# Optimization experiments

Measured on AMD Instinct MI355X. Metric: run time of the kernel, lower is better.

The kernel has to match this reference:

```python
import jax, jax.numpy as jnp
import numpy as np

D = 768
NH = 8
HD = D // NH
LAT = 64


def layernorm(x, g, b, eps=1e-5):
    mu = x.mean(-1, keepdims=True)
    var = ((x - mu) ** 2).mean(-1, keepdims=True)
    return (x - mu) * jax.lax.rsqrt(var + eps) * g + b


def mha(q, k, v, qw, qb, kw, kb, vw, vb, ow, ob):
    # torch nn.MultiheadAttention (batch_first): Linear is x @ W.T + b
    B, Lq, _ = q.shape
    qh = (q @ qw.T + qb).reshape(B, Lq, NH, HD)
    kh = (k @ kw.T + kb).reshape(B, -1, NH, HD)
    vh = (v @ vw.T + vb).reshape(B, -1, NH, HD)
    s = jnp.einsum('bqhd,bkhd->bhqk', qh, kh) * (1.0 / np.sqrt(HD))
    a = jax.nn.softmax(s, axis=-1)
    o = jnp.einsum('bhqk,bkhd->bqhd', a, vh).reshape(B, Lq, D)
    return o @ ow.T + ob


def setup_inputs() -> dict:
    key = jax.random.key(0)
    ks = jax.random.split(key, 16)
    w = lambda k, shape: (jax.random.normal(k, shape, jnp.float32) * 0.02)
    inp = {
        'frames': jax.random.normal(ks[0], (4, 4, 8, 3, 224, 224), jnp.float32),
        'pe_w': w(ks[1], (D, 3, 14, 14)), 'pe_b': jnp.zeros((D,), jnp.float32),
        'latents': jax.random.normal(ks[2], (LAT, D), jnp.float32),
        'ca_qw': w(ks[3], (D, D)), 'ca_qb': jnp.zeros((D,), jnp.float32),
        'ca_kw': w(ks[4], (D, D)), 'ca_kb': jnp.zeros((D,), jnp.float32),
        'ca_vw': w(ks[5], (D, D)), 'ca_vb': jnp.zeros((D,), jnp.float32),
        'ca_ow': w(ks[6], (D, D)), 'ca_ob': jnp.zeros((D,), jnp.float32),
        'nq_g': jnp.ones((D,), jnp.float32), 'nq_b': jnp.zeros((D,), jnp.float32),
        'nkv_g': jnp.ones((D,), jnp.float32), 'nkv_b': jnp.zeros((D,), jnp.float32),
        'no_g': jnp.ones((D,), jnp.float32), 'no_b': jnp.zeros((D,), jnp.float32),
        'm1_w': w(ks[7], (4 * D, D)), 'm1_b': jnp.zeros((4 * D,), jnp.float32),
        'm2_w': w(ks[8], (D, 4 * D)), 'm2_b': jnp.zeros((D,), jnp.float32),
        'sa_qw': w(ks[9], (D, D)), 'sa_qb': jnp.zeros((D,), jnp.float32),
        'sa_kw': w(ks[10], (D, D)), 'sa_kb': jnp.zeros((D,), jnp.float32),
        'sa_vw': w(ks[11], (D, D)), 'sa_vb': jnp.zeros((D,), jnp.float32),
        'sa_ow': w(ks[12], (D, D)), 'sa_ob': jnp.zeros((D,), jnp.float32),
        'f1_w': w(ks[13], (2 * D, D)), 'f1_b': jnp.zeros((2 * D,), jnp.float32),
        'f2_w': w(ks[14], (D, 2 * D)), 'f2_b': jnp.zeros((D,), jnp.float32),
        'n1_g': jnp.ones((D,), jnp.float32), 'n1_b': jnp.zeros((D,), jnp.float32),
        'n2_g': jnp.ones((D,), jnp.float32), 'n2_b': jnp.zeros((D,), jnp.float32),
    }
    return inp


def reference(frames, pe_w, pe_b, latents, ca_qw, ca_qb, ca_kw, ca_kb, ca_vw, ca_vb,
              ca_ow, ca_ob, nq_g, nq_b, nkv_g, nkv_b, no_g, no_b, m1_w, m1_b, m2_w, m2_b,
              sa_qw, sa_qb, sa_kw, sa_kb, sa_vw, sa_vb, sa_ow, sa_ob, f1_w, f1_b,
              f2_w, f2_b, n1_g, n1_b, n2_g, n2_b):
    B, S, T, C, H, W = frames.shape
    # --- patch embed (Conv2d k=14 s=14), batched over all seconds & frames ---
    f = frames.reshape(B * S * T, C, H, W)
    p = jax.lax.conv_general_dilated(
        f, pe_w, window_strides=(14, 14), padding='VALID',
        dimension_numbers=('NCHW', 'OIHW', 'NCHW')) + pe_b[None, :, None, None]
    npatch = p.shape[2] * p.shape[3]  # 256 patches per frame
    p = p.reshape(B * S * T, D, npatch).transpose(0, 2, 1)  # [BST, P, D]
    kv = p.reshape(B * S, T * npatch, D)  # per-second patch tokens
    # --- Perceiver second tokenizer (loop over seconds == batched over B*S) ---
    q = jnp.broadcast_to(latents[None], (B * S, LAT, D))
    out = mha(layernorm(q, nq_g, nq_b), layernorm(kv, nkv_g, nkv_b), kv,
              ca_qw, ca_qb, ca_kw, ca_kb, ca_vw, ca_vb, ca_ow, ca_ob)
    h = layernorm(out, no_g, no_b)
    tok = out + (jax.nn.gelu(h @ m1_w.T + m1_b) @ m2_w.T + m2_b)
    # concat second tokens along time
    x = tok.reshape(B, S * LAT, D)
    # --- temporal_agg: TransformerEncoderLayer (post-norm, relu, eval mode) ---
    attn = mha(x, x, x, sa_qw, sa_qb, sa_kw, sa_kb, sa_vw, sa_vb, sa_ow, sa_ob)
    x = layernorm(x + attn, n1_g, n1_b)
    ff = jax.nn.relu(x @ f1_w.T + f1_b) @ f2_w.T + f2_b
    x = layernorm(x + ff, n2_g, n2_b)
    return x
```

## Files before the change

### kernel.cpp

```cpp
#include <hip/hip_runtime.h>
#include <hip/hip_bf16.h>
#include <math.h>

typedef __hip_bfloat16 bf16;
typedef __attribute__((ext_vector_type(8))) short short8;
typedef __attribute__((ext_vector_type(4))) short short4v;
typedef __attribute__((ext_vector_type(4))) float f32x4;

__device__ __forceinline__ void gload16(const bf16* g, bf16* l) {
  __builtin_amdgcn_global_load_lds((const __attribute__((address_space(1))) void*)(g),
                                   (__attribute__((address_space(3))) void*)(l), 16, 0, 0);
}
__device__ __forceinline__ float bfu2f(unsigned short u) {
  union { unsigned u; float f; } c; c.u = ((unsigned)u) << 16; return c.f;
}
__device__ __forceinline__ short bf2s(float v) {
  union { bf16 h; short s; } c; c.h = __float2bfloat16(v); return c.s;
}
__device__ __forceinline__ short4v packbf4(f32x4 v) {
  short4v o;
  o[0] = bf2s(v[0]); o[1] = bf2s(v[1]); o[2] = bf2s(v[2]); o[3] = bf2s(v[3]);
  return o;
}

struct Seg { const float* src; bf16* dst; int rows, sc, dc; const float* scale; };
struct Segs { Seg s[13]; };

__global__ __launch_bounds__(256) void preproc_kernel(
    Segs segs,
    const float* __restrict__ frames, bf16* __restrict__ imcol,
    const float* __restrict__ kw, const float* __restrict__ nkv_g,
    const float* __restrict__ nkv_b, const float* __restrict__ kb,
    float* __restrict__ s1, float* __restrict__ s2,
    const float* __restrict__ latents, const float* __restrict__ nq_g,
    const float* __restrict__ nq_b, bf16* __restrict__ q_ln,
    const float* __restrict__ ba, const float* __restrict__ bb,
    const float* __restrict__ bc, float* __restrict__ sab_cat) {
  __shared__ float red[16];
  int b = blockIdx.x, tid = threadIdx.x;
  if (b < 29952) {
    Seg sg = segs.s[b / 2304];
    int bx = b % 2304;
    long long total = (long long)sg.rows * sg.dc;
    for (long long idx = (long long)bx * 256 + tid; idx < total; idx += 2304LL * 256) {
      int r = (int)(idx / sg.dc), c = (int)(idx % sg.dc);
      float v = (c < sg.sc) ? sg.src[(long long)r * sg.sc + c] : 0.f;
      if (sg.scale && c < sg.sc) v *= sg.scale[c];
      sg.dst[idx] = __float2bfloat16(v);
    }
  } else if (b < 40192) {
    unsigned idx8 = (unsigned)(b - 29952) * 256u + tid;
    unsigned m = idx8 / 80u;
    unsigned k0 = (idx8 % 80u) * 8u;
    unsigned n = m >> 8;
    unsigned p = m & 255u;
    unsigned py = p >> 4, px = p & 15u;
    const float* fb = frames + ((size_t)n * 3u) * 224u * 224u +
                      (size_t)py * 14u * 224u + px * 14u;
    short8 o;
    #pragma unroll
    for (int e = 0; e < 8; ++e) {
      unsigned k = k0 + e;
      float v = 0.f;
      if (k < 588u) {
        unsigned c = k / 196u, r = k % 196u;
        unsigned i = r / 14u, j = r % 14u;
        v = fb[((size_t)c * 224u + i) * 224u + j];
      }
      o[e] = bf2s(v);
    }
    *(short8*)(imcol + (size_t)m * 640u + k0) = o;
  } else if (b < 40960) {
    int j = b - 40192;
    const float* wr_ = kw + (size_t)j * 768;
    float a = 0.f, c = 0.f;
    #pragma unroll
    for (int i = 0; i < 3; ++i) {
      int d = tid + i * 256;
      float wv = wr_[d];
      a += wv * nkv_g[d];
      c += wv * nkv_b[d];
    }
    for (int off = 32; off; off >>= 1) { a += __shfl_down(a, off); c += __shfl_down(c, off); }
    int w = tid >> 6;
    if ((tid & 63) == 0) { red[w] = a; red[8 + w] = c; }
    __syncthreads();
    if (tid == 0) {
      s1[j] = red[0] + red[1] + red[2] + red[3];
      s2[j] = red[8] + red[9] + red[10] + red[11] + kb[j];
    }
  } else if (b < 41088) {
    int row = b - 40960;
    size_t base = (size_t)row * 768;
    if (row >= 64) {
      for (int i = 0; i < 3; ++i) q_ln[base + tid + i * 256] = __float2bfloat16(0.f);
      return;
    }
    float x[3];
    for (int i = 0; i < 3; ++i) x[i] = latents[base + tid + i * 256];
    float s = x[0] + x[1] + x[2];
    float sq = x[0] * x[0] + x[1] * x[1] + x[2] * x[2];
    for (int off = 32; off; off >>= 1) {
      s += __shfl_down(s, off);
      sq += __shfl_down(sq, off);
    }
    int w = tid >> 6;
    if ((tid & 63) == 0) { red[w] = s; red[4 + w] = sq; }
    __syncthreads();
    if (tid == 0) {
      red[0] = red[0] + red[1] + red[2] + red[3];
      red[4] = red[4] + red[5] + red[6] + red[7];
    }
    __syncthreads();
    float mean = red[0] * (1.f / 768.f);
    float var = red[4] * (1.f / 768.f) - mean * mean;
    float rs = rsqrtf(var + 1e-5f);
    for (int i = 0; i < 3; ++i) {
      int c = tid + i * 256;
      q_ln[base + c] = __float2bfloat16((x[i] - mean) * rs * nq_g[c] + nq_b[c]);
    }
  } else {
    int i = (b - 41088) * 256 + tid;
    if (i < 2304)
      sab_cat[i] = i < 768 ? ba[i] : (i < 1536 ? bb[i - 768] : bc[i - 1536]);
  }
}

__global__ __launch_bounds__(256) void rowstats_kernel(const bf16* __restrict__ x,
                                                       float* __restrict__ mu,
                                                       float* __restrict__ rs) {
  int row = blockIdx.x * 4 + (threadIdx.x >> 6);
  int lane = threadIdx.x & 63;
  const unsigned short* p = (const unsigned short*)(x + (size_t)row * 768);
  float s = 0.f, sq = 0.f;
  #pragma unroll
  for (int i = 0; i < 3; ++i) {
    ushort4 v = *(const ushort4*)(p + lane * 4 + i * 256);
    float f0 = bfu2f(v.x), f1 = bfu2f(v.y), f2 = bfu2f(v.z), f3 = bfu2f(v.w);
    s += f0 + f1 + f2 + f3;
    sq += f0 * f0 + f1 * f1 + f2 * f2 + f3 * f3;
  }
  for (int off = 32; off; off >>= 1) { s += __shfl_down(s, off); sq += __shfl_down(sq, off); }
  if (lane == 0) {
    float m = s * (1.f / 768.f);
    float var = sq * (1.f / 768.f) - m * m;
    mu[row] = m;
    rs[row] = rsqrtf(var + 1e-5f);
  }
}

__global__ __launch_bounds__(256) void ln_kernel(const float* __restrict__ inF,
                                                 const bf16* __restrict__ inB,
                                                 const float* __restrict__ g,
                                                 const float* __restrict__ b,
                                                 float* __restrict__ outF,
                                                 bf16* __restrict__ outB,
                                                 int validRows) {
  int row = blockIdx.x;
  int tid = threadIdx.x;
  __shared__ float red[8];
  size_t base = (size_t)row * 768;
  if (row >= validRows) {
    for (int i = 0; i < 3; ++i) {
      int c = tid + i * 256;
      if (outB) outB[base + c] = __float2bfloat16(0.f);
      if (outF) outF[base + c] = 0.f;
    }
    return;
  }
  float x[3];
  for (int i = 0; i < 3; ++i) {
    int c = tid + i * 256;
    x[i] = inF ? inF[base + c] : __bfloat162float(inB[base + c]);
  }
  float s = x[0] + x[1] + x[2];
  float sq = x[0] * x[0] + x[1] * x[1] + x[2] * x[2];
  for (int off = 32; off; off >>= 1) {
    s += __shfl_down(s, off);
    sq += __shfl_down(sq, off);
  }
  int w = tid >> 6;
  if ((tid & 63) == 0) { red[w] = s; red[4 + w] = sq; }
  __syncthreads();
  if (tid == 0) {
    red[0] = red[0] + red[1] + red[2] + red[3];
    red[4] = red[4] + red[5] + red[6] + red[7];
  }
  __syncthreads();
  float mean = red[0] * (1.f / 768.f);
  float var = red[4] * (1.f / 768.f) - mean * mean;
  float rs = rsqrtf(var + 1e-5f);
  for (int i = 0; i < 3; ++i) {
    int c = tid + i * 256;
    float y = (x[i] - mean) * rs * g[c] + b[c];
    if (outF) outF[base + c] = y;
    if (outB) outB[base + c] = __float2bfloat16(y);
  }
}

__global__ __launch_bounds__(512, 2) void gemm256(
    const bf16* __restrict__ A, const bf16* __restrict__ Bw,
    const float* __restrict__ bias,
    bf16* __restrict__ outB,
    int M, int N, int K, int act,
    const float* __restrict__ rowMu, const float* __restrict__ rowRs,
    const float* __restrict__ s1, const float* __restrict__ s2,
    bf16* __restrict__ outB2) {
  __shared__ __align__(16) bf16 As[4][8192];
  __shared__ __align__(16) bf16 Bs[4][8192];
  int tid = threadIdx.x;
  int nwg = gridDim.x * gridDim.y;
  int orig = blockIdx.y * gridDim.x + blockIdx.x;
  int xcd = orig & 7, loc = orig >> 3;
  int qq = nwg >> 3, rr = nwg & 7;
  int swz = (xcd < rr) ? (xcd * (qq + 1) + loc) : (rr * (qq + 1) + (xcd - rr) * qq + loc);
  int m0 = (swz / gridDim.x) * 256, n0 = (swz % gridDim.x) * 256;

  int lane = tid & 63, w = tid >> 6;
  int wr = w >> 2, wc = w & 3;
  int l15 = lane & 15, lq = lane >> 4;

  f32x4 acc[8][4] = {};

  #define STAGEH(buf, kt, part)                                                \
    {                                                                          \
      int koct_ = w >> 1;                                                      \
      int row0_ = (w & 1) * 64 + ((part) & 1) * 128;                           \
      if ((part) < 2)                                                          \
        gload16(A + (size_t)(m0 + row0_ + lane) * K + (kt) + koct_ * 8,        \
                &As[buf][(koct_ * 256 + row0_) * 8]);                          \
      else                                                                     \
        gload16(Bw + (size_t)(n0 + row0_ + lane) * K + (kt) + koct_ * 8,       \
                &Bs[buf][(koct_ * 256 + row0_) * 8]);                          \
    }

  int T = K >> 5;
  #pragma unroll
  for (int p = 0; p < 4; ++p) STAGEH(0, 0, p);
  #pragma unroll
  for (int p = 0; p < 4; ++p) STAGEH(1, 32, p);
  STAGEH(2, 64, 0);
  STAGEH(2, 64, 1);
  asm volatile("s_waitcnt vmcnt(6)" ::: "memory");
  __builtin_amdgcn_s_barrier();

  for (int t = 0; t < T; ++t) {
    int bufc = t & 3, bufn2 = (t + 2) & 3, bufn3 = (t + 3) & 3;
    int kt2 = (t + 2) << 5, kt3 = (t + 3) << 5;
    short8 af[4], bfr[4];
    #pragma unroll
    for (int ni = 0; ni < 4; ++ni)
      bfr[ni] = *(const short8*)(&Bs[bufc][(lq * 256 + wc * 64 + ni * 16 + l15) * 8]);
    #pragma unroll
    for (int mi = 0; mi < 4; ++mi)
      af[mi] = *(const short8*)(&As[bufc][(lq * 256 + wr * 128 + mi * 16 + l15) * 8]);
    if (t + 2 < T) { STAGEH(bufn2, kt2, 2); STAGEH(bufn2, kt2, 3); }
    __builtin_amdgcn_s_barrier();
    asm volatile("" ::: "memory");
    __builtin_amdgcn_s_setprio(1);
    #pragma unroll
    for (int mi = 0; mi < 4; ++mi)
      #pragma unroll
      for (int ni = 0; ni < 4; ++ni)
        acc[mi][ni] = __builtin_amdgcn_mfma_f32_16x16x32_bf16(bfr[ni], af[mi],
                                                              acc[mi][ni], 0, 0, 0);
    __builtin_amdgcn_s_setprio(0);
    asm volatile("" ::: "memory");
    __builtin_amdgcn_s_barrier();
    #pragma unroll
    for (int mi = 0; mi < 4; ++mi)
      af[mi] = *(const short8*)(&As[bufc][(lq * 256 + wr * 128 + 64 + mi * 16 + l15) * 8]);
    if (t + 3 < T) { STAGEH(bufn3, kt3, 0); STAGEH(bufn3, kt3, 1); }
    if (t + 3 < T) {
      asm volatile("s_waitcnt vmcnt(6)" ::: "memory");
    } else if (t + 2 < T) {
      asm volatile("s_waitcnt vmcnt(4)" ::: "memory");
    } else if (t + 1 < T) {
      asm volatile("s_waitcnt vmcnt(0)" ::: "memory");
    }
    __builtin_amdgcn_s_barrier();
    asm volatile("" ::: "memory");
    __builtin_amdgcn_s_setprio(1);
    #pragma unroll
    for (int mi = 0; mi < 4; ++mi)
      #pragma unroll
      for (int ni = 0; ni < 4; ++ni)
        acc[4 + mi][ni] = __builtin_amdgcn_mfma_f32_16x16x32_bf16(bfr[ni], af[mi],
                                                                  acc[4 + mi][ni], 0, 0, 0);
    __builtin_amdgcn_s_setprio(0);
    asm volatile("" ::: "memory");
    __builtin_amdgcn_s_barrier();
  }
  #undef STAGEH

  bf16* ldsflat = (bf16*)As;
  bf16* ep = ldsflat + w * 1152;
  int rlo = lane >> 3, cg = lane & 7;

  if (act == 3) {
    int c0w = n0 + wc * 64;
    bool isV = (c0w < 768);
    bf16* dst = isV ? outB : outB2;
    int colbase = isV ? c0w : (c0w - 768);
    f32x4 bv[4], a1[4], a2[4];
    #pragma unroll
    for (int ni = 0; ni < 4; ++ni) {
      int cc = colbase + ni * 16 + lq * 4;
      if (isV) bv[ni] = *(const f32x4*)(bias + cc);
      else { a1[ni] = *(const f32x4*)(s1 + cc); a2[ni] = *(const f32x4*)(s2 + cc); }
    }
    #pragma unroll
    for (int mi = 0; mi < 8; ++mi) {
      int roww = m0 + wr * 128 + mi * 16 + l15;
      float rs_ = 0.f, mu_ = 0.f;
      if (!isV) { rs_ = rowRs[roww]; mu_ = rowMu[roww]; }
      #pragma unroll
      for (int ni = 0; ni < 4; ++ni) {
        f32x4 v;
        if (isV) v = acc[mi][ni] + bv[ni];
        else {
          #pragma unroll
          for (int j = 0; j < 4; ++j)
            v[j] = rs_ * (acc[mi][ni][j] - mu_ * a1[ni][j]) + a2[ni][j];
        }
        *(short4v*)(ep + l15 * 72 + ni * 16 + lq * 4) = packbf4(v);
      }
      asm volatile("s_waitcnt lgkmcnt(0)" ::: "memory");
      #pragma unroll
      for (int p = 0; p < 2; ++p) {
        int r = p * 8 + rlo;
        short8 d = *(const short8*)(ep + r * 72 + cg * 8);
        int rg = m0 + wr * 128 + mi * 16 + r;
        *(short8*)(dst + (size_t)rg * 768 + colbase + cg * 8) = d;
      }
      asm volatile("s_waitcnt lgkmcnt(0)" ::: "memory");
    }
    return;
  }

  {
    int c0w = n0 + wc * 64;
    f32x4 bv[4] = {};
    if (bias) {
      #pragma unroll
      for (int ni = 0; ni < 4; ++ni)
        bv[ni] = *(const f32x4*)(bias + c0w + ni * 16 + lq * 4);
    }
    #pragma unroll
    for (int mi = 0; mi < 8; ++mi) {
      #pragma unroll
      for (int ni = 0; ni < 4; ++ni) {
        f32x4 v = acc[mi][ni] + bv[ni];
        *(short4v*)(ep + l15 * 72 + ni * 16 + lq * 4) = packbf4(v);
      }
      asm volatile("s_waitcnt lgkmcnt(0)" ::: "memory");
      #pragma unroll
      for (int p = 0; p < 2; ++p) {
        int r = p * 8 + rlo;
        short8 d = *(const short8*)(ep + r * 72 + cg * 8);
        int rg = m0 + wr * 128 + mi * 16 + r;
        *(short8*)(outB + (size_t)rg * N + c0w + cg * 8) = d;
      }
      asm volatile("s_waitcnt lgkmcnt(0)" ::: "memory");
    }
  }
}

__global__ __launch_bounds__(256) void gemm_bf16(
    const bf16* __restrict__ A, const bf16* __restrict__ Bw,
    const float* __restrict__ bias, const float* __restrict__ resid,
    float* __restrict__ outF, bf16* __restrict__ outB,
    int M, int N, int K, int act) {
  __shared__ __align__(16) bf16 As[2][4096];
  __shared__ __align__(16) bf16 Bs[2][4096];
  int tid = threadIdx.x;
  int nwg = gridDim.x * gridDim.y;
  int orig = blockIdx.y * gridDim.x + blockIdx.x;
  int xcd = orig & 7, loc = orig >> 3;
  int qq = nwg >> 3, rr = nwg & 7;
  int swz = (xcd < rr) ? (xcd * (qq + 1) + loc) : (rr * (qq + 1) + (xcd - rr) * qq + loc);
  int m0 = (swz / gridDim.x) * 128, n0 = (swz % gridDim.x) * 128;

  int lane = tid & 63, w = tid >> 6;
  int wr = w >> 1, wc = w & 1;
  int l15 = lane & 15, lq = lane >> 4;
  const bf16* Abase = A + (size_t)m0 * K + w * 8;
  const bf16* Bbase = Bw + (size_t)n0 * K + w * 8;
  f32x4 acc[4][4] = {};

  int nt = K >> 5;
  #pragma unroll
  for (int i = 0; i < 2; ++i) {
    int r = i * 64 + lane;
    gload16(Abase + (size_t)r * K, &As[0][(w * 2 + i) * 512]);
    gload16(Bbase + (size_t)r * K, &Bs[0][(w * 2 + i) * 512]);
  }
  for (int t = 0; t < nt; ++t) {
    int cur = t & 1;
    if (t + 1 < nt) {
      int kt = (t + 1) << 5;
      #pragma unroll
      for (int i = 0; i < 2; ++i) {
        int r = i * 64 + lane;
        gload16(Abase + (size_t)r * K + kt, &As[cur ^ 1][(w * 2 + i) * 512]);
        gload16(Bbase + (size_t)r * K + kt, &Bs[cur ^ 1][(w * 2 + i) * 512]);
      }
      asm volatile("s_waitcnt vmcnt(4)" ::: "memory");
    } else {
      asm volatile("s_waitcnt vmcnt(0)" ::: "memory");
    }
    __builtin_amdgcn_s_barrier();
    asm volatile("" ::: "memory");
    const bf16* Ab = &As[cur][lq * 1024];
    const bf16* Bb = &Bs[cur][lq * 1024];
    short8 af[4], bfr[4];
    #pragma unroll
    for (int mi = 0; mi < 4; ++mi)
      af[mi] = *(const short8*)(Ab + (wr * 64 + mi * 16 + l15) * 8);
    #pragma unroll
    for (int ni = 0; ni < 4; ++ni)
      bfr[ni] = *(const short8*)(Bb + (wc * 64 + ni * 16 + l15) * 8);
    __builtin_amdgcn_s_setprio(1);
    #pragma unroll
    for (int mi = 0; mi < 4; ++mi)
      #pragma unroll
      for (int ni = 0; ni < 4; ++ni)
        acc[mi][ni] = __builtin_amdgcn_mfma_f32_16x16x32_bf16(bfr[ni], af[mi],
                                                              acc[mi][ni], 0, 0, 0);
    __builtin_amdgcn_s_setprio(0);
    asm volatile("" ::: "memory");
    __builtin_amdgcn_s_barrier();
  }

  #pragma unroll
  for (int ni = 0; ni < 4; ++ni) {
    int c0 = n0 + wc * 64 + ni * 16 + lq * 4;
    f32x4 bv = {};
    if (bias) bv = *(const f32x4*)(bias + c0);
    #pragma unroll
    for (int mi = 0; mi < 4; ++mi) {
      int row = m0 + wr * 64 + mi * 16 + l15;
      f32x4 v = acc[mi][ni] + bv;
      if (act == 1) {
        #pragma unroll
        for (int j = 0; j < 4; ++j) {
          float x = v[j];
          v[j] = 0.5f * x * (1.f + tanhf(0.79788456080286535f * (x + 0.044715f * x * x * x)));
        }
      } else if (act == 2) {
        #pragma unroll
        for (int j = 0; j < 4; ++j) v[j] = fmaxf(v[j], 0.f);
      }
      size_t idx = (size_t)row * N + c0;
      if (resid) v += *(const f32x4*)(resid + idx);
      if (outF) *(f32x4*)(outF + idx) = v;
      if (outB) *(short4v*)(outB + idx) = packbf4(v);
    }
  }
}

__global__ __launch_bounds__(256) void flash_kernel(
    const bf16* __restrict__ Q, const bf16* __restrict__ Kp,
    const bf16* __restrict__ V, bf16* __restrict__ O,
    int Lk, int qRPB, int kRPB, int oRPB, int ld) {
  const float scale = 0.10206207261596575f;
  __shared__ bf16 Vt[96 * 72];
  __shared__ bf16 Ps[4 * 16 * 72];
  int tid = threadIdx.x, lane = tid & 63, w = tid >> 6;
  int l15 = lane & 15, lq = lane >> 4;
  int b = blockIdx.z, h = blockIdx.y, qt = blockIdx.x;
  int qbase = b * qRPB + qt * 64 + w * 16;
  int kbase = b * kRPB;
  int obase = b * oRPB + qt * 64 + w * 16;
  int ch = h * 96;

  short8 aQ[3];
  #pragma unroll
  for (int kd = 0; kd < 3; ++kd)
    aQ[kd] = *(const short8*)(Q + (size_t)(qbase + l15) * ld + ch + kd * 32 + lq * 8);

  f32x4 oacc[6] = {};
  float mrun[4] = {-1e30f, -1e30f, -1e30f, -1e30f};
  float lrun[4] = {0.f, 0.f, 0.f, 0.f};

  for (int kc = 0; kc < Lk; kc += 64) {
    for (int u = tid; u < 768; u += 256) {
      int kk = u / 12, dc = u % 12;
      short8 v = *(const short8*)(V + (size_t)(kbase + kc + kk) * ld + ch + dc * 8);
      const bf16* pv = (const bf16*)&v;
      #pragma unroll
      for (int e = 0; e < 8; ++e) Vt[(dc * 8 + e) * 72 + kk] = pv[e];
    }
    __syncthreads();

    f32x4 sacc[4] = {};
    #pragma unroll
    for (int ni = 0; ni < 4; ++ni)
      #pragma unroll
      for (int kd = 0; kd < 3; ++kd) {
        short8 bK = *(const short8*)(Kp + (size_t)(kbase + kc + ni * 16 + l15) * ld +
                                     ch + kd * 32 + lq * 8);
        sacc[ni] = __builtin_amdgcn_mfma_f32_16x16x32_bf16(aQ[kd], bK, sacc[ni], 0, 0, 0);
      }
    #pragma unroll
    for (int ni = 0; ni < 4; ++ni)
      #pragma unroll
      for (int j = 0; j < 4; ++j) sacc[ni][j] *= scale;

    float al[4];
    #pragma unroll
    for (int j = 0; j < 4; ++j) {
      float mx = fmaxf(fmaxf(sacc[0][j], sacc[1][j]), fmaxf(sacc[2][j], sacc[3][j]));
      #pragma unroll
      for (int off = 1; off < 16; off <<= 1) mx = fmaxf(mx, __shfl_xor(mx, off));
      float mnew = fmaxf(mrun[j], mx);
      float alpha = __expf(mrun[j] - mnew);
      float rsum = 0.f;
      #pragma unroll
      for (int ni = 0; ni < 4; ++ni) {
        float p = __expf(sacc[ni][j] - mnew);
        sacc[ni][j] = p;
        rsum += p;
      }
      #pragma unroll
      for (int off = 1; off < 16; off <<= 1) rsum += __shfl_xor(rsum, off);
      lrun[j] = lrun[j] * alpha + rsum;
      mrun[j] = mnew;
      al[j] = alpha;
    }

    #pragma unroll
    for (int ni = 0; ni < 4; ++ni)
      #pragma unroll
      for (int j = 0; j < 4; ++j)
        Ps[(w * 16 + lq * 4 + j) * 72 + ni * 16 + l15] = __float2bfloat16(sacc[ni][j]);
    #pragma unroll
    for (int t = 0; t < 6; ++t)
      #pragma unroll
      for (int j = 0; j < 4; ++j) oacc[t][j] *= al[j];
    short8 aP[2];
    #pragma unroll
    for (int ks = 0; ks < 2; ++ks)
      aP[ks] = *(const short8*)(&Ps[(w * 16 + l15) * 72 + ks * 32 + lq * 8]);
    #pragma unroll
    for (int t = 0; t < 6; ++t)
      #pragma unroll
      for (int ks = 0; ks < 2; ++ks) {
        short8 bV = *(const short8*)(&Vt[(t * 16 + l15) * 72 + ks * 32 + lq * 8]);
        oacc[t] = __builtin_amdgcn_mfma_f32_16x16x32_bf16(aP[ks], bV, oacc[t], 0, 0, 0);
      }
    __syncthreads();
  }

  #pragma unroll
  for (int t = 0; t < 6; ++t)
    #pragma unroll
    for (int j = 0; j < 4; ++j) {
      int row = obase + lq * 4 + j;
      int col = ch + t * 16 + l15;
      O[(size_t)row * 768 + col] = __float2bfloat16(oacc[t][j] / lrun[j]);
    }
}

__global__ __launch_bounds__(256) void flash_split_kernel(
    const bf16* __restrict__ Q, const bf16* __restrict__ Kp,
    const bf16* __restrict__ V, float* __restrict__ Opart,
    float* __restrict__ Mpart, float* __restrict__ Lpart,
    int splitLen, int kRPB) {
  const float scale = 0.10206207261596575f;
  __shared__ bf16 Vt[96 * 72];
  __shared__ bf16 Ps[4 * 16 * 72];
  int tid = threadIdx.x, lane = tid & 63, w = tid >> 6;
  int l15 = lane & 15, lq = lane >> 4;
  int s = blockIdx.x, h = blockIdx.y, b = blockIdx.z;
  int kbase = b * kRPB + s * splitLen;
  int ch = h * 96;

  short8 aQ[3];
  #pragma unroll
  for (int kd = 0; kd < 3; ++kd)
    aQ[kd] = *(const short8*)(Q + (size_t)(w * 16 + l15) * 768 + ch + kd * 32 + lq * 8);

  f32x4 oacc[6] = {};
  float mrun[4] = {-1e30f, -1e30f, -1e30f, -1e30f};
  float lrun[4] = {0.f, 0.f, 0.f, 0.f};

  for (int kc = 0; kc < splitLen; kc += 64) {
    for (int u = tid; u < 768; u += 256) {
      int kk = u / 12, dc = u % 12;
      short8 v = *(const short8*)(V + (size_t)(kbase + kc + kk) * 768 + ch + dc * 8);
      const bf16* pv = (const bf16*)&v;
      #pragma unroll
      for (int e = 0; e < 8; ++e) Vt[(dc * 8 + e) * 72 + kk] = pv[e];
    }
    __syncthreads();

    f32x4 sacc[4] = {};
    #pragma unroll
    for (int ni = 0; ni < 4; ++ni)
      #pragma unroll
      for (int kd = 0; kd < 3; ++kd) {
        short8 bK = *(const short8*)(Kp + (size_t)(kbase + kc + ni * 16 + l15) * 768 +
                                     ch + kd * 32 + lq * 8);
        sacc[ni] = __builtin_amdgcn_mfma_f32_16x16x32_bf16(aQ[kd], bK, sacc[ni], 0, 0, 0);
      }
    #pragma unroll
    for (int ni = 0; ni < 4; ++ni)
      #pragma unroll
      for (int j = 0; j < 4; ++j) sacc[ni][j] *= scale;

    float al[4];
    #pragma unroll
    for (int j = 0; j < 4; ++j) {
      float mx = fmaxf(fmaxf(sacc[0][j], sacc[1][j]), fmaxf(sacc[2][j], sacc[3][j]));
      #pragma unroll
      for (int off = 1; off < 16; off <<= 1) mx = fmaxf(mx, __shfl_xor(mx, off));
      float mnew = fmaxf(mrun[j], mx);
      float alpha = __expf(mrun[j] - mnew);
      float rsum = 0.f;
      #pragma unroll
      for (int ni = 0; ni < 4; ++ni) {
        float p = __expf(sacc[ni][j] - mnew);
        sacc[ni][j] = p;
        rsum += p;
      }
      #pragma unroll
      for (int off = 1; off < 16; off <<= 1) rsum += __shfl_xor(rsum, off);
      lrun[j] = lrun[j] * alpha + rsum;
      mrun[j] = mnew;
      al[j] = alpha;
    }

    #pragma unroll
    for (int ni = 0; ni < 4; ++ni)
      #pragma unroll
      for (int j = 0; j < 4; ++j)
        Ps[(w * 16 + lq * 4 + j) * 72 + ni * 16 + l15] = __float2bfloat16(sacc[ni][j]);
    #pragma unroll
    for (int t = 0; t < 6; ++t)
      #pragma unroll
      for (int j = 0; j < 4; ++j) oacc[t][j] *= al[j];
    short8 aP[2];
    #pragma unroll
    for (int ks = 0; ks < 2; ++ks)
      aP[ks] = *(const short8*)(&Ps[(w * 16 + l15) * 72 + ks * 32 + lq * 8]);
    #pragma unroll
    for (int t = 0; t < 6; ++t)
      #pragma unroll
      for (int ks = 0; ks < 2; ++ks) {
        short8 bV = *(const short8*)(&Vt[(t * 16 + l15) * 72 + ks * 32 + lq * 8]);
        oacc[t] = __builtin_amdgcn_mfma_f32_16x16x32_bf16(aP[ks], bV, oacc[t], 0, 0, 0);
      }
    __syncthreads();
  }

  int orow = b * 64 + w * 16;
  #pragma unroll
  for (int t = 0; t < 6; ++t)
    #pragma unroll
    for (int j = 0; j < 4; ++j)
      Opart[(size_t)(s * 1024 + orow + lq * 4 + j) * 768 + ch + t * 16 + l15] = oacc[t][j];
  if (l15 == 0) {
    #pragma unroll
    for (int j = 0; j < 4; ++j) {
      int qqi = w * 16 + lq * 4 + j;
      int mi = ((s * 16 + b) * 8 + h) * 64 + qqi;
      Mpart[mi] = mrun[j];
      Lpart[mi] = lrun[j];
    }
  }
}

__global__ __launch_bounds__(256) void flash_merge_kernel(
    const float* __restrict__ Opart, const float* __restrict__ Mpart,
    const float* __restrict__ Lpart, bf16* __restrict__ O, int nsplit) {
  int row = blockIdx.x;
  int tid = threadIdx.x;
  int c0 = tid * 3;
  int b = row >> 6, q = row & 63;
  int h = c0 / 96;
  float m = -1e30f;
  for (int s = 0; s < nsplit; ++s)
    m = fmaxf(m, Mpart[((s * 16 + b) * 8 + h) * 64 + q]);
  float l = 0.f, o0 = 0.f, o1 = 0.f, o2 = 0.f;
  for (int s = 0; s < nsplit; ++s) {
    int mi = ((s * 16 + b) * 8 + h) * 64 + q;
    float ws = __expf(Mpart[mi] - m);
    l += ws * Lpart[mi];
    const float* op = Opart + (size_t)(s * 1024 + row) * 768 + c0;
    o0 += ws * op[0]; o1 += ws * op[1]; o2 += ws * op[2];
  }
  float inv = 1.f / l;
  size_t ob = (size_t)row * 768 + c0;
  O[ob]     = __float2bfloat16(o0 * inv);
  O[ob + 1] = __float2bfloat16(o1 * inv);
  O[ob + 2] = __float2bfloat16(o2 * inv);
}

extern "C" void kernel_launch(void* const* d_in, const int* in_sizes, int n_in,
                              void* d_out, int out_size, void* d_ws, size_t ws_size,
                              hipStream_t stream) {
  const float* frames = (const float*)d_in[0];
  const float* pe_w   = (const float*)d_in[1];
  const float* pe_b   = (const float*)d_in[2];
  const float* latents= (const float*)d_in[3];
  const float* ca_qw  = (const float*)d_in[4];  const float* ca_qb = (const float*)d_in[5];
  const float* ca_kw  = (const float*)d_in[6];  const float* ca_kb = (const float*)d_in[7];
  const float* ca_vw  = (const float*)d_in[8];  const float* ca_vb = (const float*)d_in[9];
  const float* ca_ow  = (const float*)d_in[10]; const float* ca_ob = (const float*)d_in[11];
  const float* nq_g   = (const float*)d_in[12]; const float* nq_b  = (const float*)d_in[13];
  const float* nkv_g  = (const float*)d_in[14]; const float* nkv_b = (const float*)d_in[15];
  const float* no_g   = (const float*)d_in[16]; const float* no_b  = (const float*)d_in[17];
  const float* m1_w   = (const float*)d_in[18]; const float* m1_b  = (const float*)d_in[19];
  const float* m2_w   = (const float*)d_in[20]; const float* m2_b  = (const float*)d_in[21];
  const float* sa_qw  = (const float*)d_in[22]; const float* sa_qb = (const float*)d_in[23];
  const float* sa_kw  = (const float*)d_in[24]; const float* sa_kb = (const float*)d_in[25];
  const float* sa_vw  = (const float*)d_in[26]; const float* sa_vb = (const float*)d_in[27];
  const float* sa_ow  = (const float*)d_in[28]; const float* sa_ob = (const float*)d_in[29];
  const float* f1_w   = (const float*)d_in[30]; const float* f1_b  = (const float*)d_in[31];
  const float* f2_w   = (const float*)d_in[32]; const float* f2_b  = (const float*)d_in[33];
  const float* n1_g   = (const float*)d_in[34]; const float* n1_b  = (const float*)d_in[35];
  const float* n2_g   = (const float*)d_in[36]; const float* n2_b  = (const float*)d_in[37];

  char* ws = (char*)d_ws;
  size_t off = 0;
  auto take = [&](size_t bytes) -> char* {
    char* p = ws + off;
    off += (bytes + 255) & ~(size_t)255;
    return p;
  };

  bf16* w_pe   = (bf16*)take((size_t)768 * 640 * 2);
  bf16* w_caq  = (bf16*)take((size_t)768 * 768 * 2);
  bf16* w_cakv = (bf16*)take((size_t)1536 * 768 * 2);
  bf16* w_cao  = (bf16*)take((size_t)768 * 768 * 2);
  bf16* w_m1   = (bf16*)take((size_t)3072 * 768 * 2);
  bf16* w_m2   = (bf16*)take((size_t)768 * 3072 * 2);
  bf16* w_saq  = (bf16*)take((size_t)768 * 768 * 2);
  bf16* w_sak  = (bf16*)take((size_t)768 * 768 * 2);
  bf16* w_sav  = (bf16*)take((size_t)768 * 768 * 2);
  bf16* w_sao  = (bf16*)take((size_t)768 * 768 * 2);
  bf16* w_f1   = (bf16*)take((size_t)1536 * 768 * 2);
  bf16* w_f2   = (bf16*)take((size_t)768 * 1536 * 2);
  float* sab_cat = (float*)take((size_t)2304 * 4);
  float* s1v  = (float*)take((size_t)768 * 4);
  float* s2v  = (float*)take((size_t)768 * 4);
  float* muv  = (float*)take((size_t)32768 * 4);
  float* rsv  = (float*)take((size_t)32768 * 4);

  bf16* q_ln = (bf16*)take((size_t)128 * 768 * 2);
  bf16* qh   = (bf16*)take((size_t)128 * 768 * 2);

  bf16* kv   = (bf16*)take((size_t)32768 * 768 * 2);
  bf16* vhkh = (bf16*)take((size_t)2 * 32768 * 768 * 2);
  bf16* vh = vhkh;
  bf16* kh = vhkh + (size_t)32768 * 768;
  bf16* imcol = vhkh;

  const size_t REGION = (size_t)32768 * 608 * 2;
  char* region = take(REGION);
  float* Opart = (float*)region;
  float* Mpart = (float*)(region + 25165824);
  float* Lpart = (float*)(region + 25165824 + 262144);
  bf16*  attn_o = (bf16*)(region + REGION - (size_t)1024 * 768 * 2);
  size_t ro = 0;
  auto rtake = [&](size_t bytes) -> char* {
    char* p = region + ro;
    ro += (bytes + 255) & ~(size_t)255;
    return p;
  };
  float* out_f  = (float*)rtake((size_t)1024 * 768 * 4);
  bf16*  h_b    = (bf16*)rtake((size_t)1024 * 768 * 2);
  bf16*  g_b    = (bf16*)rtake((size_t)1024 * 3072 * 2);
  float* tok_f  = (float*)rtake((size_t)1024 * 768 * 4);
  bf16*  tok_b  = (bf16*)rtake((size_t)1024 * 768 * 2);
  bf16*  xqkv   = (bf16*)rtake((size_t)1024 * 2304 * 2);
  bf16*  sa_o   = (bf16*)rtake((size_t)1024 * 768 * 2);
  float* y_f    = (float*)rtake((size_t)1024 * 768 * 4);
  float* x1f    = (float*)rtake((size_t)1024 * 768 * 4);
  bf16*  x1b    = (bf16*)rtake((size_t)1024 * 768 * 2);
  bf16*  ff1    = (bf16*)rtake((size_t)1024 * 1536 * 2);
  float* z_f    = (float*)rtake((size_t)1024 * 768 * 4);
  (void)ws_size; (void)in_sizes; (void)n_in; (void)out_size;

  Segs segs;
  segs.s[0]  = {pe_w,  w_pe,  768, 588, 640, nullptr};
  segs.s[1]  = {ca_qw, w_caq, 768, 768, 768, nullptr};
  segs.s[2]  = {ca_vw, w_cakv, 768, 768, 768, nullptr};
  segs.s[3]  = {ca_kw, w_cakv + (size_t)768 * 768, 768, 768, 768, nkv_g};
  segs.s[4]  = {ca_ow, w_cao, 768, 768, 768, nullptr};
  segs.s[5]  = {m1_w,  w_m1,  3072, 768, 768, nullptr};
  segs.s[6]  = {m2_w,  w_m2,  768, 3072, 3072, nullptr};
  segs.s[7]  = {sa_qw, w_saq, 768, 768, 768, nullptr};
  segs.s[8]  = {sa_kw, w_sak, 768, 768, 768, nullptr};
  segs.s[9]  = {sa_vw, w_sav, 768, 768, 768, nullptr};
  segs.s[10] = {f1_w,  w_f1,  1536, 768, 768, nullptr};
  segs.s[11] = {f2_w,  w_f2,  768, 1536, 1536, nullptr};
  segs.s[12] = {sa_ow, w_sao, 768, 768, 768, nullptr};
  preproc_kernel<<<41097, 256, 0, stream>>>(
      segs, frames, imcol,
      ca_kw, nkv_g, nkv_b, ca_kb, s1v, s2v,
      latents, nq_g, nq_b, q_ln,
      sa_qb, sa_kb, sa_vb, sab_cat);

  gemm256<<<dim3(3, 128), 512, 0, stream>>>(imcol, w_pe, pe_b, kv,
                                            32768, 768, 640, 0,
                                            nullptr, nullptr, nullptr, nullptr, nullptr);

  gemm_bf16<<<dim3(6, 1), 256, 0, stream>>>(q_ln, w_caq, ca_qb, nullptr, nullptr, qh,
                                            128, 768, 768, 0);

  rowstats_kernel<<<8192, 256, 0, stream>>>(kv, muv, rsv);

  gemm256<<<dim3(6, 128), 512, 0, stream>>>(kv, w_cakv, ca_vb, vh,
                                            32768, 1536, 768, 3,
                                            muv, rsv, s1v, s2v, kh);

  flash_split_kernel<<<dim3(8, 8, 16), 256, 0, stream>>>(qh, kh, vh, Opart, Mpart, Lpart,
                                                         256, 2048);
  flash_merge_kernel<<<1024, 256, 0, stream>>>(Opart, Mpart, Lpart, attn_o, 8);

  gemm_bf16<<<dim3(6, 8), 256, 0, stream>>>(attn_o, w_cao, ca_ob, nullptr, out_f, nullptr,
                                            1024, 768, 768, 0);

  ln_kernel<<<1024, 256, 0, stream>>>(out_f, nullptr, no_g, no_b, nullptr, h_b, 1024);

  gemm_bf16<<<dim3(24, 8), 256, 0, stream>>>(h_b, w_m1, m1_b, nullptr, nullptr, g_b,
                                             1024, 3072, 768, 1);

  gemm_bf16<<<dim3(6, 8), 256, 0, stream>>>(g_b, w_m2, m2_b, out_f, tok_f, tok_b,
                                            1024, 768, 3072, 0);

  gemm_bf16<<<dim3(18, 8), 256, 0, stream>>>(tok_b, w_saq, sab_cat, nullptr, nullptr, xqkv,
                                             1024, 2304, 768, 0);

  flash_kernel<<<dim3(4, 8, 4), 256, 0, stream>>>(xqkv, xqkv + 768, xqkv + 1536, sa_o,
                                                  256, 256, 256, 256, 2304);

  gemm_bf16<<<dim3(6, 8), 256, 0, stream>>>(sa_o, w_sao, sa_ob, tok_f, y_f, nullptr,
                                            1024, 768, 768, 0);

  ln_kernel<<<1024, 256, 0, stream>>>(y_f, nullptr, n1_g, n1_b, x1f, x1b, 1024);

  gemm_bf16<<<dim3(12, 8), 256, 0, stream>>>(x1b, w_f1, f1_b, nullptr, nullptr, ff1,
                                             1024, 1536, 768, 2);

  gemm_bf16<<<dim3(6, 8), 256, 0, stream>>>(ff1, w_f2, f2_b, x1f, z_f, nullptr,
                                            1024, 768, 1536, 0);

  ln_kernel<<<1024, 256, 0, stream>>>(z_f, nullptr, n2_g, n2_b, (float*)d_out, nullptr, 1024);
}
```

Baseline: 676.5 us.

## Fold LayerNorms into following GEMM epilogues and halve flash split partial precision

Removes two standalone LayerNorm kernels. Gamma is folded into the MLP and FFN weights, with precomputed column sums s1/s2. Row mean and rstd come from a lightweight rowstats pass, and the normalization is applied inside the GEMM epilogue (new act modes 4/5/6); the residual LN is recomputed in the f2 epilogue. Separately, cross-attention now uses 16 splits of 128 instead of 8 of 256, with bf16 partial outputs, to add parallelism and cut merge traffic at some accuracy risk. Row stats taken from bf16 copies rather than fp32 add small numerical error.

```diff
diff --git a/kernel.cpp b/kernel.cpp
--- a/kernel.cpp
+++ b/kernel.cpp
@@ -21,6 +21,9 @@
   short4v o;
   o[0] = bf2s(v[0]); o[1] = bf2s(v[1]); o[2] = bf2s(v[2]); o[3] = bf2s(v[3]);
   return o;
+}
+__device__ __forceinline__ float geluf(float x) {
+  return 0.5f * x * (1.f + tanhf(0.79788456080286535f * (x + 0.044715f * x * x * x)));
 }
 
 struct Seg { const float* src; bf16* dst; int rows, sc, dc; const float* scale; };
@@ -35,7 +38,13 @@
     const float* __restrict__ latents, const float* __restrict__ nq_g,
     const float* __restrict__ nq_b, bf16* __restrict__ q_ln,
     const float* __restrict__ ba, const float* __restrict__ bb,
-    const float* __restrict__ bc, float* __restrict__ sab_cat) {
+    const float* __restrict__ bc, float* __restrict__ sab_cat,
+    const float* __restrict__ m1w, const float* __restrict__ no_g,
+    const float* __restrict__ no_b, const float* __restrict__ m1b,
+    float* __restrict__ s1m, float* __restrict__ s2m,
+    const float* __restrict__ f1w, const float* __restrict__ n1_g,
+    const float* __restrict__ n1_b, const float* __restrict__ f1b,
+    float* __restrict__ s1f, float* __restrict__ s2f) {
   __shared__ float red[16];
   int b = blockIdx.x, tid = threadIdx.x;
   if (b < 29952) {
@@ -48,7 +57,9 @@
       if (sg.scale && c < sg.sc) v *= sg.scale[c];
       sg.dst[idx] = __float2bfloat16(v);
     }
-  } else if (b < 40192) {
+    return;
+  }
+  if (b < 40192) {
     unsigned idx8 = (unsigned)(b - 29952) * 256u + tid;
     unsigned m = idx8 / 80u;
     unsigned k0 = (idx8 % 80u) * 8u;
@@ -70,25 +81,13 @@
       o[e] = bf2s(v);
     }
     *(short8*)(imcol + (size_t)m * 640u + k0) = o;
-  } else if (b < 40960) {
-    int j = b - 40192;
-    const float* wr_ = kw + (size_t)j * 768;
-    float a = 0.f, c = 0.f;
-    #pragma unroll
-    for (int i = 0; i < 3; ++i) {
-      int d = tid + i * 256;
-      float wv = wr_[d];
-      a += wv * nkv_g[d];
-      c += wv * nkv_b[d];
-    }
-    for (int off = 32; off; off >>= 1) { a += __shfl_down(a, off); c += __shfl_down(c, off); }
-    int w = tid >> 6;
-    if ((tid & 63) == 0) { red[w] = a; red[8 + w] = c; }
-    __syncthreads();
-    if (tid == 0) {
-      s1[j] = red[0] + red[1] + red[2] + red[3];
-      s2[j] = red[8] + red[9] + red[10] + red[11] + kb[j];
-    }
+    return;
+  }
+  const float* wsrc = nullptr; const float* gv = nullptr; const float* bv = nullptr;
+  const float* bias = nullptr; float* o1 = nullptr; float* o2 = nullptr;
+  int j = -1;
+  if (b < 40960) {
+    j = b - 40192; wsrc = kw; gv = nkv_g; bv = nkv_b; bias = kb; o1 = s1; o2 = s2;
   } else if (b < 41088) {
     int row = b - 40960;
     size_t base = (size_t)row * 768;
@@ -119,10 +118,35 @@
       int c = tid + i * 256;
       q_ln[base + c] = __float2bfloat16((x[i] - mean) * rs * nq_g[c] + nq_b[c]);
     }
-  } else {
+    return;
+  } else if (b < 41097) {
     int i = (b - 41088) * 256 + tid;
     if (i < 2304)
       sab_cat[i] = i < 768 ? ba[i] : (i < 1536 ? bb[i - 768] : bc[i - 1536]);
+    return;
+  } else if (b < 44169) {
+    j = b - 41097; wsrc = m1w; gv = no_g; bv = no_b; bias = m1b; o1 = s1m; o2 = s2m;
+  } else {
+    j = b - 44169; wsrc = f1w; gv = n1_g; bv = n1_b; bias = f1b; o1 = s1f; o2 = s2f;
+  }
+  {
+    const float* wr_ = wsrc + (size_t)j * 768;
+    float a = 0.f, c = 0.f;
+    #pragma unroll
+    for (int i = 0; i < 3; ++i) {
+      int d = tid + i * 256;
+      float wv = wr_[d];
+      a += wv * gv[d];
+      c += wv * bv[d];
+    }
+    for (int off = 32; off; off >>= 1) { a += __shfl_down(a, off); c += __shfl_down(c, off); }
+    int w = tid >> 6;
+    if ((tid & 63) == 0) { red[w] = a; red[8 + w] = c; }
+    __syncthreads();
+    if (tid == 0) {
+      o1[j] = red[0] + red[1] + red[2] + red[3];
+      o2[j] = red[8] + red[9] + red[10] + red[11] + bias[j];
+    }
   }
 }
 
@@ -150,29 +174,15 @@
 }
 
 __global__ __launch_bounds__(256) void ln_kernel(const float* __restrict__ inF,
-                                                 const bf16* __restrict__ inB,
                                                  const float* __restrict__ g,
                                                  const float* __restrict__ b,
-                                                 float* __restrict__ outF,
-                                                 bf16* __restrict__ outB,
-                                                 int validRows) {
+                                                 float* __restrict__ outF) {
   int row = blockIdx.x;
   int tid = threadIdx.x;
   __shared__ float red[8];
   size_t base = (size_t)row * 768;
-  if (row >= validRows) {
-    for (int i = 0; i < 3; ++i) {
-      int c = tid + i * 256;
-      if (outB) outB[base + c] = __float2bfloat16(0.f);
-      if (outF) outF[base + c] = 0.f;
-    }
-    return;
-  }
   float x[3];
-  for (int i = 0; i < 3; ++i) {
-    int c = tid + i * 256;
-    x[i] = inF ? inF[base + c] : __bfloat162float(inB[base + c]);
-  }
+  for (int i = 0; i < 3; ++i) x[i] = inF[base + tid + i * 256];
   float s = x[0] + x[1] + x[2];
   float sq = x[0] * x[0] + x[1] * x[1] + x[2] * x[2];
   for (int off = 32; off; off >>= 1) {
@@ -192,9 +202,7 @@
   float rs = rsqrtf(var + 1e-5f);
   for (int i = 0; i < 3; ++i) {
     int c = tid + i * 256;
-    float y = (x[i] - mean) * rs * g[c] + b[c];
-    if (outF) outF[base + c] = y;
-    if (outB) outB[base + c] = __float2bfloat16(y);
+    outF[base + c] = (x[i] - mean) * rs * g[c] + b[c];
   }
 }
 
@@ -370,7 +378,11 @@
     const bf16* __restrict__ A, const bf16* __restrict__ Bw,
     const float* __restrict__ bias, const float* __restrict__ resid,
     float* __restrict__ outF, bf16* __restrict__ outB,
-    int M, int N, int K, int act) {
+    int M, int N, int K, int act,
+    const float* __restrict__ rowMu, const float* __restrict__ rowRs,
+    const float* __restrict__ s1, const float* __restrict__ s2,
+    const float* __restrict__ yraw, const float* __restrict__ gamma,
+    const float* __restrict__ beta) {
   __shared__ __align__(16) bf16 As[2][4096];
   __shared__ __align__(16) bf16 Bs[2][4096];
   int tid = threadIdx.x;
@@ -432,6 +444,50 @@
     __builtin_amdgcn_s_barrier();
   }
 
+  if (act == 4 || act == 5) {
+    #pragma unroll
+    for (int ni = 0; ni < 4; ++ni) {
+      int c0 = n0 + wc * 64 + ni * 16 + lq * 4;
+      f32x4 a1 = *(const f32x4*)(s1 + c0);
+      f32x4 a2 = *(const f32x4*)(s2 + c0);
+      #pragma unroll
+      for (int mi = 0; mi < 4; ++mi) {
+        int row = m0 + wr * 64 + mi * 16 + l15;
+        float rs_ = rowRs[row], mu_ = rowMu[row];
+        f32x4 v;
+        #pragma unroll
+        for (int j = 0; j < 4; ++j) {
+          float x = rs_ * (acc[mi][ni][j] - mu_ * a1[j]) + a2[j];
+          v[j] = (act == 4) ? geluf(x) : fmaxf(x, 0.f);
+        }
+        *(short4v*)(outB + (size_t)row * N + c0) = packbf4(v);
+      }
+    }
+    return;
+  }
+  if (act == 6) {
+    #pragma unroll
+    for (int ni = 0; ni < 4; ++ni) {
+      int c0 = n0 + wc * 64 + ni * 16 + lq * 4;
+      f32x4 bv = *(const f32x4*)(bias + c0);
+      f32x4 gm = *(const f32x4*)(gamma + c0);
+      f32x4 bt = *(const f32x4*)(beta + c0);
+      #pragma unroll
+      for (int mi = 0; mi < 4; ++mi) {
+        int row = m0 + wr * 64 + mi * 16 + l15;
+        float rs_ = rowRs[row], mu_ = rowMu[row];
+        size_t idx = (size_t)row * N + c0;
+        f32x4 yv = *(const f32x4*)(yraw + idx);
+        f32x4 v;
+        #pragma unroll
+        for (int j = 0; j < 4; ++j)
+          v[j] = acc[mi][ni][j] + bv[j] + (rs_ * (yv[j] - mu_) * gm[j] + bt[j]);
+        *(f32x4*)(outF + idx) = v;
+      }
+    }
+    return;
+  }
+
   #pragma unroll
   for (int ni = 0; ni < 4; ++ni) {
     int c0 = n0 + wc * 64 + ni * 16 + lq * 4;
@@ -443,10 +499,7 @@
       f32x4 v = acc[mi][ni] + bv;
       if (act == 1) {
         #pragma unroll
-        for (int j = 0; j < 4; ++j) {
-          float x = v[j];
-          v[j] = 0.5f * x * (1.f + tanhf(0.79788456080286535f * (x + 0.044715f * x * x * x)));
-        }
+        for (int j = 0; j < 4; ++j) v[j] = geluf(v[j]);
       } else if (act == 2) {
         #pragma unroll
         for (int j = 0; j < 4; ++j) v[j] = fmaxf(v[j], 0.f);
@@ -564,9 +617,9 @@
 
 __global__ __launch_bounds__(256) void flash_split_kernel(
     const bf16* __restrict__ Q, const bf16* __restrict__ Kp,
-    const bf16* __restrict__ V, float* __restrict__ Opart,
+    const bf16* __restrict__ V, bf16* __restrict__ Opart,
     float* __restrict__ Mpart, float* __restrict__ Lpart,
-    int splitLen, int kRPB) {
+    int splitLen, int kRPB, int nsplit) {
   const float scale = 0.10206207261596575f;
   __shared__ bf16 Vt[96 * 72];
   __shared__ bf16 Ps[4 * 16 * 72];
@@ -659,7 +712,8 @@
   for (int t = 0; t < 6; ++t)
     #pragma unroll
     for (int j = 0; j < 4; ++j)
-      Opart[(size_t)(s * 1024 + orow + lq * 4 + j) * 768 + ch + t * 16 + l15] = oacc[t][j];
+      Opart[(size_t)(s * 1024 + orow + lq * 4 + j) * 768 + ch + t * 16 + l15] =
+          __float2bfloat16(oacc[t][j]);
   if (l15 == 0) {
     #pragma unroll
     for (int j = 0; j < 4; ++j) {
@@ -672,7 +726,7 @@
 }
 
 __global__ __launch_bounds__(256) void flash_merge_kernel(
-    const float* __restrict__ Opart, const float* __restrict__ Mpart,
+    const bf16* __restrict__ Opart, const float* __restrict__ Mpart,
     const float* __restrict__ Lpart, bf16* __restrict__ O, int nsplit) {
   int row = blockIdx.x;
   int tid = threadIdx.x;
@@ -683,12 +737,15 @@
   for (int s = 0; s < nsplit; ++s)
     m = fmaxf(m, Mpart[((s * 16 + b) * 8 + h) * 64 + q]);
   float l = 0.f, o0 = 0.f, o1 = 0.f, o2 = 0.f;
+  const unsigned short* opu = (const unsigned short*)Opart;
   for (int s = 0; s < nsplit; ++s) {
     int mi = ((s * 16 + b) * 8 + h) * 64 + q;
     float ws = __expf(Mpart[mi] - m);
     l += ws * Lpart[mi];
-    const float* op = Opart + (size_t)(s * 1024 + row) * 768 + c0;
-    o0 += ws * op[0]; o1 += ws * op[1]; o2 += ws * op[2];
+    size_t ob = (size_t)(s * 1024 + row) * 768 + c0;
+    o0 += ws * bfu2f(opu[ob]);
+    o1 += ws * bfu2f(opu[ob + 1]);
+    o2 += ws * bfu2f(opu[ob + 2]);
   }
   float inv = 1.f / l;
   size_t ob = (size_t)row * 768 + c0;
@@ -745,8 +802,16 @@
   float* sab_cat = (float*)take((size_t)2304 * 4);
   float* s1v  = (float*)take((size_t)768 * 4);
   float* s2v  = (float*)take((size_t)768 * 4);
+  float* s1m  = (float*)take((size_t)3072 * 4);
+  float* s2m  = (float*)take((size_t)3072 * 4);
+  float* s1f  = (float*)take((size_t)1536 * 4);
+  float* s2f  = (float*)take((size_t)1536 * 4);
   float* muv  = (float*)take((size_t)32768 * 4);
   float* rsv  = (float*)take((size_t)32768 * 4);
+  float* muo  = (float*)take((size_t)1024 * 4);
+  float* rso  = (float*)take((size_t)1024 * 4);
+  float* muy  = (float*)take((size_t)1024 * 4);
+  float* rsy  = (float*)take((size_t)1024 * 4);
 
   bf16* q_ln = (bf16*)take((size_t)128 * 768 * 2);
   bf16* qh   = (bf16*)take((size_t)128 * 768 * 2);
@@ -759,9 +824,9 @@
 
   const size_t REGION = (size_t)32768 * 608 * 2;
   char* region = take(REGION);
-  float* Opart = (float*)region;
+  bf16*  Opart = (bf16*)region;
   float* Mpart = (float*)(region + 25165824);
-  float* Lpart = (float*)(region + 25165824 + 262144);
+  float* Lpart = (float*)(region + 25165824 + 524288);
   bf16*  attn_o = (bf16*)(region + REGION - (size_t)1024 * 768 * 2);
   size_t ro = 0;
   auto rtake = [&](size_t bytes) -> char* {
@@ -770,15 +835,14 @@
     return p;
   };
   float* out_f  = (float*)rtake((size_t)1024 * 768 * 4);
-  bf16*  h_b    = (bf16*)rtake((size_t)1024 * 768 * 2);
+  bf16*  out_b  = (bf16*)rtake((size_t)1024 * 768 * 2);
   bf16*  g_b    = (bf16*)rtake((size_t)1024 * 3072 * 2);
   float* tok_f  = (float*)rtake((size_t)1024 * 768 * 4);
   bf16*  tok_b  = (bf16*)rtake((size_t)1024 * 768 * 2);
   bf16*  xqkv   = (bf16*)rtake((size_t)1024 * 2304 * 2);
   bf16*  sa_o   = (bf16*)rtake((size_t)1024 * 768 * 2);
   float* y_f    = (float*)rtake((size_t)1024 * 768 * 4);
-  float* x1f    = (float*)rtake((size_t)1024 * 768 * 4);
-  bf16*  x1b    = (bf16*)rtake((size_t)1024 * 768 * 2);
+  bf16*  y_b    = (bf16*)rtake((size_t)1024 * 768 * 2);
   bf16*  ff1    = (bf16*)rtake((size_t)1024 * 1536 * 2);
   float* z_f    = (float*)rtake((size_t)1024 * 768 * 4);
   (void)ws_size; (void)in_sizes; (void)n_in; (void)out_size;
@@ -789,26 +853,30 @@
   segs.s[2]  = {ca_vw, w_cakv, 768, 768, 768, nullptr};
   segs.s[3]  = {ca_kw, w_cakv + (size_t)768 * 768, 768, 768, 768, nkv_g};
   segs.s[4]  = {ca_ow, w_cao, 768, 768, 768, nullptr};
-  segs.s[5]  = {m1_w,  w_m1,  3072, 768, 768, nullptr};
+  segs.s[5]  = {m1_w,  w_m1,  3072, 768, 768, no_g};
   segs.s[6]  = {m2_w,  w_m2,  768, 3072, 3072, nullptr};
   segs.s[7]  = {sa_qw, w_saq, 768, 768, 768, nullptr};
   segs.s[8]  = {sa_kw, w_sak, 768, 768, 768, nullptr};
   segs.s[9]  = {sa_vw, w_sav, 768, 768, 768, nullptr};
-  segs.s[10] = {f1_w,  w_f1,  1536, 768, 768, nullptr};
+  segs.s[10] = {f1_w,  w_f1,  1536, 768, 768, n1_g};
   segs.s[11] = {f2_w,  w_f2,  768, 1536, 1536, nullptr};
   segs.s[12] = {sa_ow, w_sao, 768, 768, 768, nullptr};
-  preproc_kernel<<<41097, 256, 0, stream>>>(
+  preproc_kernel<<<45705, 256, 0, stream>>>(
       segs, frames, imcol,
       ca_kw, nkv_g, nkv_b, ca_kb, s1v, s2v,
       latents, nq_g, nq_b, q_ln,
-      sa_qb, sa_kb, sa_vb, sab_cat);
+      sa_qb, sa_kb, sa_vb, sab_cat,
+      m1_w, no_g, no_b, m1_b, s1m, s2m,
+      f1_w, n1_g, n1_b, f1_b, s1f, s2f);
 
   gemm256<<<dim3(3, 128), 512, 0, stream>>>(imcol, w_pe, pe_b, kv,
                                             32768, 768, 640, 0,
                                             nullptr, nullptr, nullptr, nullptr, nullptr);
 
   gemm_bf16<<<dim3(6, 1), 256, 0, stream>>>(q_ln, w_caq, ca_qb, nullptr, nullptr, qh,
-                                            128, 768, 768, 0);
+                                            128, 768, 768, 0,
+                                            nullptr, nullptr, nullptr, nullptr,
+                                            nullptr, nullptr, nullptr);
 
   rowstats_kernel<<<8192, 256, 0, stream>>>(kv, muv, rsv);
 
@@ -816,37 +884,49 @@
                                             32768, 1536, 768, 3,
                                             muv, rsv, s1v, s2v, kh);
 
-  flash_split_kernel<<<dim3(8, 8, 16), 256, 0, stream>>>(qh, kh, vh, Opart, Mpart, Lpart,
-                                                         256, 2048);
-  flash_merge_kernel<<<1024, 256, 0, stream>>>(Opart, Mpart, Lpart, attn_o, 8);
-
-  gemm_bf16<<<dim3(6, 8), 256, 0, stream>>>(attn_o, w_cao, ca_ob, nullptr, out_f, nullptr,
-                                            1024, 768, 768, 0);
-
-  ln_kernel<<<1024, 256, 0, stream>>>(out_f, nullptr, no_g, no_b, nullptr, h_b, 1024);
-
-  gemm_bf16<<<dim3(24, 8), 256, 0, stream>>>(h_b, w_m1, m1_b, nullptr, nullptr, g_b,
-                                             1024, 3072, 768, 1);
+  flash_split_kernel<<<dim3(16, 8, 16), 256, 0, stream>>>(qh, kh, vh, Opart, Mpart, Lpart,
+                                                          128, 2048, 16);
+  flash_merge_kernel<<<1024, 256, 0, stream>>>(Opart, Mpart, Lpart, attn_o, 16);
+
+  gemm_bf16<<<dim3(6, 8), 256, 0, stream>>>(attn_o, w_cao, ca_ob, nullptr, out_f, out_b,
+                                            1024, 768, 768, 0,
+                                            nullptr, nullptr, nullptr, nullptr,
+                                            nullptr, nullptr, nullptr);
+  rowstats_kernel<<<256, 256, 0, stream>>>(out_b, muo, rso);
+
+  gemm_bf16<<<dim3(24, 8), 256, 0, stream>>>(out_b, w_m1, nullptr, nullptr, nullptr, g_b,
+                                             1024, 3072, 768, 4,
+                                             muo, rso, s1m, s2m,
+                                             nullptr, nullptr, nullptr);
 
   gemm_bf16<<<dim3(6, 8), 256, 0, stream>>>(g_b, w_m2, m2_b, out_f, tok_f, tok_b,
-                                            1024, 768, 3072, 0);
+                                            1024, 768, 3072, 0,
+                                            nullptr, nullptr, nullptr, nullptr,
+                                            nullptr, nullptr, nullptr);
 
   gemm_bf16<<<dim3(18, 8), 256, 0, stream>>>(tok_b, w_saq, sab_cat, nullptr, nullptr, xqkv,
-                                             1024, 2304, 768, 0);
+                                             1024, 2304, 768, 0,
+                                             nullptr, nullptr, nullptr, nullptr,
+                                             nullptr, nullptr, nullptr);
 
   flash_kernel<<<dim3(4, 8, 4), 256, 0, stream>>>(xqkv, xqkv + 768, xqkv + 1536, sa_o,
                                                   256, 256, 256, 256, 2304);
 
-  gemm_bf16<<<dim3(6, 8), 256, 0, stream>>>(sa_o, w_sao, sa_ob, tok_f, y_f, nullptr,
-                                            1024, 768, 768, 0);
-
-  ln_kernel<<<1024, 256, 0, stream>>>(y_f, nullptr, n1_g, n1_b, x1f, x1b, 1024);
-
-  gemm_bf16<<<dim3(12, 8), 256, 0, stream>>>(x1b, w_f1, f1_b, nullptr, nullptr, ff1,
-                                             1024, 1536, 768, 2);
-
-  gemm_bf16<<<dim3(6, 8), 256, 0, stream>>>(ff1, w_f2, f2_b, x1f, z_f, nullptr,
-                                            1024, 768, 1536, 0);
-
-  ln_kernel<<<1024, 256, 0, stream>>>(z_f, nullptr, n2_g, n2_b, (float*)d_out, nullptr, 1024);
-}
+  gemm_bf16<<<dim3(6, 8), 256, 0, stream>>>(sa_o, w_sao, sa_ob, tok_f, y_f, y_b,
+                                            1024, 768, 768, 0,
+                                            nullptr, nullptr, nullptr, nullptr,
+                                            nullptr, nullptr, nullptr);
+  rowstats_kernel<<<256, 256, 0, stream>>>(y_b, muy, rsy);
+
+  gemm_bf16<<<dim3(12, 8), 256, 0, stream>>>(y_b, w_f1, nullptr, nullptr, nullptr, ff1,
+                                             1024, 1536, 768, 5,
+                                             muy, rsy, s1f, s2f,
+                                             nullptr, nullptr, nullptr);
+
+  gemm_bf16<<<dim3(6, 8), 256, 0, stream>>>(ff1, w_f2, f2_b, nullptr, z_f, nullptr,
+                                            1024, 768, 1536, 6,
+                                            muy, rsy, nullptr, nullptr,
+                                            y_f, n1_g, n1_b);
+
+  ln_kernel<<<1024, 256, 0, stream>>>(z_f, n2_g, n2_b, (float*)d_out);
+}
```

Result: no change. 685.4 us (+1.3%).
